# Kernel tuning notes

Hardware: AMD Instinct MI355X
Metric: run time of the kernel (lower is better)

The kernel has to match this reference:

```python
import jax, jax.numpy as jnp
import numpy as np

N = 100000      # num_assets (nodes)
E = 1600000     # edges (avg degree 16)
D_IN, D_H, D_OUT = 128, 64, 64


def gcn_conv(x, W, b, src, dst, dinv):
    """PyG-style GCNConv: h = D^{-1/2}(A+I)D^{-1/2} (x @ W) + b.
    Self-loop contribution handled analytically (norm = dinv[i]^2)."""
    h = x @ W                                   # [N, out]
    norm = dinv[src] * dinv[dst]                # [E]
    agg = jax.ops.segment_sum(h[src] * norm[:, None], dst, num_segments=N)
    agg = agg + h * (dinv * dinv)[:, None]      # self-loops
    return agg + b


def setup_inputs() -> dict:
    key = jax.random.key(0)
    ks = jax.random.split(key, 10)
    x = jax.random.normal(ks[0], (N, D_IN), dtype=jnp.float32)
    edge_index = jax.random.randint(ks[1], (2, E), 0, N, dtype=jnp.int64)
    s = 0.1
    W1 = jax.random.normal(ks[2], (D_IN, D_H), dtype=jnp.float32) * s
    b1 = jnp.zeros((D_H,), dtype=jnp.float32)
    W2 = jax.random.normal(ks[3], (D_H, D_H), dtype=jnp.float32) * s
    b2 = jnp.zeros((D_H,), dtype=jnp.float32)
    W3 = jax.random.normal(ks[4], (D_H, D_OUT), dtype=jnp.float32) * s
    b3 = jnp.zeros((D_OUT,), dtype=jnp.float32)
    Wa = jax.random.normal(ks[5], (D_OUT, D_OUT), dtype=jnp.float32) * s  # torch Linear weight [out,in]
    ba = jnp.zeros((D_OUT,), dtype=jnp.float32)
    q = jax.random.normal(ks[6], (D_OUT, 1), dtype=jnp.float32)
    battn = jax.random.normal(ks[7], (1,), dtype=jnp.float32)
    return {"x": x, "edge_index": edge_index, "W1": W1, "b1": b1,
            "W2": W2, "b2": b2, "W3": W3, "b3": b3,
            "Wa": Wa, "ba": ba, "q": q, "battn": battn}


def reference(x, edge_index, W1, b1, W2, b2, W3, b3, Wa, ba, q, battn):
    src, dst = edge_index[0], edge_index[1]
    # degree of A + I (computed once, shared by all layers)
    deg = jax.ops.segment_sum(jnp.ones((E,), dtype=x.dtype), dst, num_segments=N) + 1.0
    dinv = jax.lax.rsqrt(deg)

    h = jax.nn.relu(gcn_conv(x, W1, b1, src, dst, dinv))
    h = jax.nn.relu(gcn_conv(h, W2, b2, src, dst, dinv))
    z_context = gcn_conv(h, W3, b3, src, dst, dinv)          # [N, D_OUT]

    attn_scores = jnp.tanh(z_context @ Wa.T + ba) @ q + battn  # [N, 1]
    attn = jax.nn.softmax(attn_scores, axis=0)                 # softmax over nodes
    global_context = jnp.sum(attn * z_context, axis=0)         # [D_OUT]
    return (z_context, global_context)
```

## Files before the change

kernel.cpp:

```cpp
#include <hip/hip_runtime.h>
#include <hip/hip_fp16.h>
#include <math.h>
#include <stdint.h>


__global__ void detect_i64_kernel(const int* __restrict__ ei, int* __restrict__ flag) {
    int t = threadIdx.x;
    int bad = 0;
#pragma unroll
    for (int j = 0; j < 4; j++)
        bad |= (ei[1 + 2 * (t * 4 + j)] != 0);
    unsigned long long m = __ballot(bad);
    if (t == 0) *flag = (m == 0ull) ? 1 : 0;
}

__global__ void fill_kernel(const void* __restrict__ ei, const int* __restrict__ flag,
                            int* __restrict__ cnt, int* __restrict__ buckets,
                            int CAP, int E, int lo, int hi) {
    int e = blockIdx.x * 256 + threadIdx.x;
    if (e >= E) return;
    int is64 = *flag;
    int d = is64 ? (int)((const long long*)ei)[E + e] : ((const int*)ei)[E + e];
    if (d < lo || d >= hi) return;
    int s = is64 ? (int)((const long long*)ei)[e] : ((const int*)ei)[e];
    int pos = atomicAdd(&cnt[d], 1);
    if (pos < CAP) buckets[(size_t)d * CAP + pos] = s;
}

__global__ void dinv_kernel(const int* __restrict__ cnt, float* __restrict__ dinv, int N) {
    int i = blockIdx.x * 256 + threadIdx.x;
    if (i < N) dinv[i] = rsqrtf((float)cnt[i] + 1.0f);
}

template <int K, bool PRE>
__global__ __launch_bounds__(256) void gemm64(const float* __restrict__ in,
                                              const float* __restrict__ Wg,
                                              const float* __restrict__ bias,
                                              const float* __restrict__ dinv,
                                              __half* __restrict__ outh, int nrows) {
    constexpr int KQ = K / 4;
    __shared__ float Wt[64 * K];
    __shared__ float bl[K];
    const int t  = threadIdx.x;
    const int rb = blockIdx.x * 64;

    for (int qidx = t; qidx < K * 16; qidx += 256) {
        int k  = qidx >> 4;
        int c0 = (qidx & 15) << 2;
        float4 v = *(const float4*)(Wg + k * 64 + c0);
        float vv[4] = {v.x, v.y, v.z, v.w};
#pragma unroll
        for (int j = 0; j < 4; j++) {
            int c  = c0 + j;
            int kq = (k >> 2) ^ ((c >> 2) & 7);
            Wt[(c * KQ + kq) * 4 + (k & 3)] = vv[j];
        }
    }
    if (PRE) {
        for (int idx = t; idx < K; idx += 256) bl[idx] = bias[idx];
    }
    __syncthreads();

    const int tc = t & 15;
    const int tr = t >> 4;
    int rowi[4];
#pragma unroll
    for (int i = 0; i < 4; i++) {
        int r = rb + tr * 4 + i;
        rowi[i] = (r < nrows) ? r : (nrows - 1);
    }

    float acc[4][4];
#pragma unroll
    for (int i = 0; i < 4; i++)
#pragma unroll
        for (int j = 0; j < 4; j++) acc[i][j] = 0.f;

#pragma unroll 2
    for (int kb = 0; kb < KQ; ++kb) {
        float4 a[4];
#pragma unroll
        for (int i = 0; i < 4; i++)
            a[i] = *(const float4*)(in + (size_t)rowi[i] * K + (kb << 2));
        if (PRE) {
            float4 bb = *(const float4*)(bl + (kb << 2));
#pragma unroll
            for (int i = 0; i < 4; i++) {
                a[i].x = fmaxf(a[i].x + bb.x, 0.f);
                a[i].y = fmaxf(a[i].y + bb.y, 0.f);
                a[i].z = fmaxf(a[i].z + bb.z, 0.f);
                a[i].w = fmaxf(a[i].w + bb.w, 0.f);
            }
        }
        float4 w[4];
#pragma unroll
        for (int j = 0; j < 4; j++) {
            int c = tc * 4 + j;
            w[j] = *(const float4*)(&Wt[(c * KQ + (kb ^ ((c >> 2) & 7))) * 4]);
        }
#pragma unroll
        for (int i = 0; i < 4; i++)
#pragma unroll
            for (int j = 0; j < 4; j++)
                acc[i][j] += a[i].x * w[j].x + a[i].y * w[j].y +
                             a[i].z * w[j].z + a[i].w * w[j].w;
    }
#pragma unroll
    for (int i = 0; i < 4; i++) {
        int r = rb + tr * 4 + i;
        if (r < nrows) {
            float dd = dinv[r];
            __half2 p0 = __floats2half2_rn(acc[i][0] * dd, acc[i][1] * dd);
            __half2 p1 = __floats2half2_rn(acc[i][2] * dd, acc[i][3] * dd);
            uint2 pk;
            pk.x = *(unsigned int*)&p0;
            pk.y = *(unsigned int*)&p1;
            *(uint2*)(outh + (size_t)r * 64 + tc * 4) = pk;
        }
    }
}

template <bool BIAS>
__global__ __launch_bounds__(256) void gather64(const __half* __restrict__ hs,
                                                const int* __restrict__ cnt,
                                                const int* __restrict__ buckets,
                                                int CAP,
                                                const float* __restrict__ bias,
                                                float* __restrict__ out, int N) {
    const int wid = (blockIdx.x * 256 + threadIdx.x) >> 6;
    if (wid >= N) return;
    const int lane = threadIdx.x & 63;
    const int g    = lane >> 4;
    const int q    = lane & 15;

    const int deg  = cnt[wid];
    const int degc = min(deg, CAP);
    const int* bk  = buckets + (size_t)wid * CAP;
    const int pm   = degc - 1;

    float4 acc = make_float4(0.f, 0.f, 0.f, 0.f);
    if (g == 0) {
        uint2 v = *(const uint2*)(hs + (size_t)wid * 64 + q * 4);
        float2 f0 = __half22float2(*(__half2*)&v.x);
        float2 f1 = __half22float2(*(__half2*)&v.y);
        acc = make_float4(f0.x, f0.y, f1.x, f1.y);
    }

    for (int base = 0; base < degc; base += 16) {
        int i0 = base + g;
        int i1 = i0 + 4;
        int i2 = i0 + 8;
        int i3 = i0 + 12;
        int s0 = bk[i0 <= pm ? i0 : pm];
        int s1 = bk[i1 <= pm ? i1 : pm];
        int s2 = bk[i2 <= pm ? i2 : pm];
        int s3 = bk[i3 <= pm ? i3 : pm];
        uint2 v0 = *(const uint2*)(hs + (size_t)s0 * 64 + q * 4);
        uint2 v1 = *(const uint2*)(hs + (size_t)s1 * 64 + q * 4);
        uint2 v2 = *(const uint2*)(hs + (size_t)s2 * 64 + q * 4);
        uint2 v3 = *(const uint2*)(hs + (size_t)s3 * 64 + q * 4);
        float m0 = (i0 <= pm) ? 1.f : 0.f;
        float m1 = (i1 <= pm) ? 1.f : 0.f;
        float m2 = (i2 <= pm) ? 1.f : 0.f;
        float m3 = (i3 <= pm) ? 1.f : 0.f;
        float2 a0 = __half22float2(*(__half2*)&v0.x), b0 = __half22float2(*(__half2*)&v0.y);
        float2 a1 = __half22float2(*(__half2*)&v1.x), b1 = __half22float2(*(__half2*)&v1.y);
        float2 a2 = __half22float2(*(__half2*)&v2.x), b2 = __half22float2(*(__half2*)&v2.y);
        float2 a3 = __half22float2(*(__half2*)&v3.x), b3 = __half22float2(*(__half2*)&v3.y);
        acc.x = fmaf(m0, a0.x, acc.x); acc.y = fmaf(m0, a0.y, acc.y);
        acc.z = fmaf(m0, b0.x, acc.z); acc.w = fmaf(m0, b0.y, acc.w);
        acc.x = fmaf(m1, a1.x, acc.x); acc.y = fmaf(m1, a1.y, acc.y);
        acc.z = fmaf(m1, b1.x, acc.z); acc.w = fmaf(m1, b1.y, acc.w);
        acc.x = fmaf(m2, a2.x, acc.x); acc.y = fmaf(m2, a2.y, acc.y);
        acc.z = fmaf(m2, b2.x, acc.z); acc.w = fmaf(m2, b2.y, acc.w);
        acc.x = fmaf(m3, a3.x, acc.x); acc.y = fmaf(m3, a3.y, acc.y);
        acc.z = fmaf(m3, b3.x, acc.z); acc.w = fmaf(m3, b3.y, acc.w);
    }
    acc.x += __shfl_xor(acc.x, 16); acc.y += __shfl_xor(acc.y, 16);
    acc.z += __shfl_xor(acc.z, 16); acc.w += __shfl_xor(acc.w, 16);
    acc.x += __shfl_xor(acc.x, 32); acc.y += __shfl_xor(acc.y, 32);
    acc.z += __shfl_xor(acc.z, 32); acc.w += __shfl_xor(acc.w, 32);

    if (g == 0) {
        float dd = rsqrtf((float)deg + 1.0f);
        float4 o = make_float4(acc.x * dd, acc.y * dd, acc.z * dd, acc.w * dd);
        if (BIAS) {
            float4 b = *(const float4*)(bias + q * 4);
            o.x += b.x; o.y += b.y; o.z += b.z; o.w += b.w;
        }
        *(float4*)(out + (size_t)wid * 64 + q * 4) = o;
    }
}

__device__ __forceinline__ float fast_tanh(float x) {
    float e = __expf(2.f * x);
    return 1.f - 2.f * __builtin_amdgcn_rcpf(e + 1.f);
}

__global__ __launch_bounds__(256) void scoregc_kernel(const float* __restrict__ z,
                                                      const float* __restrict__ Wa,
                                                      const float* __restrict__ ba,
                                                      const float* __restrict__ q,
                                                      const float* __restrict__ battn,
                                                      float* __restrict__ blockmax,
                                                      float* __restrict__ bsumE,
                                                      float* __restrict__ bpart, int N) {
    __shared__ float Wl[64 * 64];
    __shared__ float es[256];
    __shared__ float red[256];
    __shared__ float gp[4][64];
    int t = threadIdx.x;
    for (int idx = t * 4; idx < 64 * 64; idx += 1024)
        *(float4*)(Wl + idx) = *(const float4*)(Wa + idx);
    __syncthreads();

    int i = blockIdx.x * 256 + t;
    float sc = -1e30f;
    if (i < N) {
        float zi[64];
#pragma unroll
        for (int kq = 0; kq < 16; kq++) {
            float4 v = *(const float4*)(z + (size_t)i * 64 + kq * 4);
            zi[kq * 4 + 0] = v.x; zi[kq * 4 + 1] = v.y;
            zi[kq * 4 + 2] = v.z; zi[kq * 4 + 3] = v.w;
        }
        float s = battn[0];
        for (int j = 0; j < 64; j++) {
            float t0 = ba[j], t1 = 0.f, t2 = 0.f, t3 = 0.f;
#pragma unroll
            for (int kq = 0; kq < 16; kq++) {
                float4 w4 = *(const float4*)(Wl + j * 64 + kq * 4);
                t0 = fmaf(zi[kq * 4 + 0], w4.x, t0);
                t1 = fmaf(zi[kq * 4 + 1], w4.y, t1);
                t2 = fmaf(zi[kq * 4 + 2], w4.z, t2);
                t3 = fmaf(zi[kq * 4 + 3], w4.w, t3);
            }
            s += fast_tanh((t0 + t1) + (t2 + t3)) * q[j];
        }
        sc = s;
    }
    red[t] = sc;
    __syncthreads();
    for (int off = 128; off > 0; off >>= 1) {
        if (t < off) red[t] = fmaxf(red[t], red[t + off]);
        __syncthreads();
    }
    float m_b = red[0];
    __syncthreads();
    float e = (i < N) ? __expf(sc - m_b) : 0.f;
    es[t] = e;
    red[t] = e;
    __syncthreads();
    for (int off = 128; off > 0; off >>= 1) {
        if (t < off) red[t] += red[t + off];
        __syncthreads();
    }
    if (t == 0) { bsumE[blockIdx.x] = red[0]; blockmax[blockIdx.x] = m_b; }
    int f = t & 63, g = t >> 6;
    int base = blockIdx.x * 256;
    float a = 0.f;
    for (int n = 0; n < 64; n++) {
        int idx = base + g * 64 + n;
        if (idx < N) a = fmaf(es[g * 64 + n], z[(size_t)idx * 64 + f], a);
    }
    gp[g][f] = a;
    __syncthreads();
    if (g == 0) bpart[(size_t)blockIdx.x * 64 + f] = gp[0][f] + gp[1][f] + gp[2][f] + gp[3][f];
}

__global__ __launch_bounds__(1024) void final3_kernel(const float* __restrict__ blockmax,
                                                      const float* __restrict__ bsumE,
                                                      const float* __restrict__ bpart,
                                                      int NB, float* __restrict__ outg) {
    __shared__ float sm[1024];
    __shared__ float se[1024];
    __shared__ float sa[16][64];
    int t = threadIdx.x;
    float m = -1e30f;
    for (int b = t; b < NB; b += 1024) m = fmaxf(m, blockmax[b]);
    sm[t] = m;
    __syncthreads();
    for (int off = 512; off > 0; off >>= 1) {
        if (t < off) sm[t] = fmaxf(sm[t], sm[t + off]);
        __syncthreads();
    }
    float M = sm[0];

    float es = 0.f;
    for (int b = t; b < NB; b += 1024) es += bsumE[b] * __expf(blockmax[b] - M);
    se[t] = es;
    __syncthreads();
    for (int off = 512; off > 0; off >>= 1) {
        if (t < off) se[t] += se[t + off];
        __syncthreads();
    }

    int f = t & 63, c = t >> 6;
    float a = 0.f;
    for (int b = c; b < NB; b += 16)
        a += bpart[(size_t)b * 64 + f] * __expf(blockmax[b] - M);
    sa[c][f] = a;
    __syncthreads();
    for (int off = 8; off > 0; off >>= 1) {
        if (c < off) sa[c][f] += sa[c + off][f];
        __syncthreads();
    }
    if (c == 0) outg[f] = sa[0][f] / se[0];
}

extern "C" void kernel_launch(void* const* d_in, const int* in_sizes, int n_in,
                              void* d_out, int out_size, void* d_ws, size_t ws_size,
                              hipStream_t stream) {
    const float* x     = (const float*)d_in[0];
    const void*  ei    = d_in[1];
    const float* W1    = (const float*)d_in[2];
    const float* b1    = (const float*)d_in[3];
    const float* W2    = (const float*)d_in[4];
    const float* b2    = (const float*)d_in[5];
    const float* W3    = (const float*)d_in[6];
    const float* b3    = (const float*)d_in[7];
    const float* Wa    = (const float*)d_in[8];
    const float* ba    = (const float*)d_in[9];
    const float* q     = (const float*)d_in[10];
    const float* battn = (const float*)d_in[11];

    const int N = in_sizes[0] / 128;
    const int E = in_sizes[1] / 2;

    float*  ws       = (float*)d_ws;
    float*  dinv     = ws;
    __half* H        = (__half*)(ws + N);
    float*  blockmax = ws + N + (size_t)32 * N;
    float*  bsumE    = blockmax + 512;
    float*  bpart    = bsumE + 512;
    int*    flag     = (int*)(bpart + 512 * 64);
    int*    cnt      = flag + 4;
    int*    buckets  = cnt + N;

    size_t fixed_bytes = (size_t)((char*)buckets - (char*)d_ws);
    size_t rem = (ws_size > fixed_bytes) ? (ws_size - fixed_bytes) : 0;
    size_t cap_fit = rem / ((size_t)N * sizeof(int));
    int CAP = (int)(cap_fit < 64 ? cap_fit : 64);
    if (CAP < 8) CAP = 8;

    float* Z    = (float*)d_out;
    float* outg = Z + (size_t)N * 64;

    hipMemsetAsync(cnt, 0, (size_t)N * sizeof(int), stream);
    detect_i64_kernel<<<1, 64, 0, stream>>>((const int*)ei, flag);

    const int NP = 4;
    const int rng = (N + NP - 1) / NP;
    for (int p = 0; p < NP; ++p) {
        int lo = p * rng;
        int hi = (p == NP - 1) ? N : lo + rng;
        fill_kernel<<<(E + 255) / 256, 256, 0, stream>>>(ei, flag, cnt, buckets,
                                                         CAP, E, lo, hi);
    }
    dinv_kernel<<<(N + 255) / 256, 256, 0, stream>>>(cnt, dinv, N);

    const int gb = (N + 63) / 64;
    const int ag = (int)(((long long)N * 64 + 255) / 256);
    const int NB = (N + 255) / 256;

    gemm64<128, false><<<gb, 256, 0, stream>>>(x, W1, nullptr, dinv, H, N);
    gather64<false><<<ag, 256, 0, stream>>>(H, cnt, buckets, CAP, nullptr, Z, N);

    gemm64<64, true><<<gb, 256, 0, stream>>>(Z, W2, b1, dinv, H, N);
    gather64<false><<<ag, 256, 0, stream>>>(H, cnt, buckets, CAP, nullptr, Z, N);

    gemm64<64, true><<<gb, 256, 0, stream>>>(Z, W3, b2, dinv, H, N);
    gather64<true><<<ag, 256, 0, stream>>>(H, cnt, buckets, CAP, b3, Z, N);

    scoregc_kernel<<<NB, 256, 0, stream>>>(Z, Wa, ba, q, battn,
                                           blockmax, bsumE, bpart, N);
    final3_kernel<<<1, 1024, 0, stream>>>(blockmax, bsumE, bpart, NB, outg);
}
```

Before: 367.7 us.

## Shrink attention score kernel to one wavefront per block with shuffle reductions

The attention-score and partial global-context kernel now runs 64-thread blocks (one wavefront) and replaces the shared-memory tree reductions and barriers with cross-lane shuffles. Wa is read straight from global memory, where the uniform address should hit cache, instead of being staged in LDS. This removes LDS staging and __syncthreads overhead, but quadruples the number of per-block partials that the final single-block reduction must combine. The workspace is enlarged to hold the extra partials.

```diff
diff --git a/kernel.cpp b/kernel.cpp
--- a/kernel.cpp
+++ b/kernel.cpp
@@ -197,39 +197,39 @@
     return 1.f - 2.f * __builtin_amdgcn_rcpf(e + 1.f);
 }
 
-__global__ __launch_bounds__(256) void scoregc_kernel(const float* __restrict__ z,
-                                                      const float* __restrict__ Wa,
-                                                      const float* __restrict__ ba,
-                                                      const float* __restrict__ q,
-                                                      const float* __restrict__ battn,
-                                                      float* __restrict__ blockmax,
-                                                      float* __restrict__ bsumE,
-                                                      float* __restrict__ bpart, int N) {
-    __shared__ float Wl[64 * 64];
-    __shared__ float es[256];
-    __shared__ float red[256];
-    __shared__ float gp[4][64];
-    int t = threadIdx.x;
-    for (int idx = t * 4; idx < 64 * 64; idx += 1024)
-        *(float4*)(Wl + idx) = *(const float4*)(Wa + idx);
-    __syncthreads();
-
-    int i = blockIdx.x * 256 + t;
-    float sc = -1e30f;
-    if (i < N) {
-        float zi[64];
+__global__ __launch_bounds__(64) void scoregc_kernel(const float* __restrict__ z,
+                                                     const float* __restrict__ Wa,
+                                                     const float* __restrict__ ba,
+                                                     const float* __restrict__ q,
+                                                     const float* __restrict__ battn,
+                                                     float* __restrict__ blockmax,
+                                                     float* __restrict__ bsumE,
+                                                     float* __restrict__ bpart, int N) {
+    const int t = threadIdx.x;
+    const int i = blockIdx.x * 64 + t;
+    const bool act = (i < N);
+
+    float zi[64];
+    if (act) {
 #pragma unroll
         for (int kq = 0; kq < 16; kq++) {
             float4 v = *(const float4*)(z + (size_t)i * 64 + kq * 4);
             zi[kq * 4 + 0] = v.x; zi[kq * 4 + 1] = v.y;
             zi[kq * 4 + 2] = v.z; zi[kq * 4 + 3] = v.w;
         }
+    } else {
+#pragma unroll
+        for (int k = 0; k < 64; k++) zi[k] = 0.f;
+    }
+
+    float sc = -1e30f;
+    {
         float s = battn[0];
         for (int j = 0; j < 64; j++) {
             float t0 = ba[j], t1 = 0.f, t2 = 0.f, t3 = 0.f;
 #pragma unroll
             for (int kq = 0; kq < 16; kq++) {
-                float4 w4 = *(const float4*)(Wl + j * 64 + kq * 4);
+                float4 w4 = *(const float4*)(Wa + j * 64 + kq * 4);
                 t0 = fmaf(zi[kq * 4 + 0], w4.x, t0);
                 t1 = fmaf(zi[kq * 4 + 1], w4.y, t1);
                 t2 = fmaf(zi[kq * 4 + 2], w4.z, t2);
@@ -237,35 +237,27 @@
             }
             s += fast_tanh((t0 + t1) + (t2 + t3)) * q[j];
         }
-        sc = s;
-    }
-    red[t] = sc;
-    __syncthreads();
-    for (int off = 128; off > 0; off >>= 1) {
-        if (t < off) red[t] = fmaxf(red[t], red[t + off]);
-        __syncthreads();
-    }
-    float m_b = red[0];
-    __syncthreads();
-    float e = (i < N) ? __expf(sc - m_b) : 0.f;
-    es[t] = e;
-    red[t] = e;
-    __syncthreads();
-    for (int off = 128; off > 0; off >>= 1) {
-        if (t < off) red[t] += red[t + off];
-        __syncthreads();
-    }
-    if (t == 0) { bsumE[blockIdx.x] = red[0]; blockmax[blockIdx.x] = m_b; }
-    int f = t & 63, g = t >> 6;
-    int base = blockIdx.x * 256;
+        if (act) sc = s;
+    }
+
+    float m = sc;
+#pragma unroll
+    for (int off = 32; off > 0; off >>= 1) m = fmaxf(m, __shfl_xor(m, off));
+    float e = act ? __expf(sc - m) : 0.f;
+    float se = e;
+#pragma unroll
+    for (int off = 32; off > 0; off >>= 1) se += __shfl_xor(se, off);
+    if (t == 0) { blockmax[blockIdx.x] = m; bsumE[blockIdx.x] = se; }
+
+    const int base = blockIdx.x * 64;
     float a = 0.f;
     for (int n = 0; n < 64; n++) {
-        int idx = base + g * 64 + n;
-        if (idx < N) a = fmaf(es[g * 64 + n], z[(size_t)idx * 64 + f], a);
-    }
-    gp[g][f] = a;
-    __syncthreads();
-    if (g == 0) bpart[(size_t)blockIdx.x * 64 + f] = gp[0][f] + gp[1][f] + gp[2][f] + gp[3][f];
+        float en = __shfl(e, n);
+        int idx = base + n;
+        idx = (idx < N) ? idx : (N - 1);
+        a = fmaf(en, z[(size_t)idx * 64 + t], a);
+    }
+    bpart[(size_t)blockIdx.x * 64 + t] = a;
 }
 
 __global__ __launch_bounds__(1024) void final3_kernel(const float* __restrict__ blockmax,
@@ -331,9 +323,9 @@
     float*  dinv     = ws;
     __half* H        = (__half*)(ws + N);
     float*  blockmax = ws + N + (size_t)32 * N;
-    float*  bsumE    = blockmax + 512;
-    float*  bpart    = bsumE + 512;
-    int*    flag     = (int*)(bpart + 512 * 64);
+    float*  bsumE    = blockmax + 2048;
+    float*  bpart    = bsumE + 2048;
+    int*    flag     = (int*)(bpart + 2048 * 64);
     int*    cnt      = flag + 4;
     int*    buckets  = cnt + N;
 
@@ -361,7 +353,7 @@
 
     const int gb = (N + 63) / 64;
     const int ag = (int)(((long long)N * 64 + 255) / 256);
-    const int NB = (N + 255) / 256;
+    const int NBW = (N + 63) / 64;
 
     gemm64<128, false><<<gb, 256, 0, stream>>>(x, W1, nullptr, dinv, H, N);
     gather64<false><<<ag, 256, 0, stream>>>(H, cnt, buckets, CAP, nullptr, Z, N);
@@ -372,7 +364,7 @@
     gemm64<64, true><<<gb, 256, 0, stream>>>(Z, W3, b2, dinv, H, N);
     gather64<true><<<ag, 256, 0, stream>>>(H, cnt, buckets, CAP, b3, Z, N);
 
-    scoregc_kernel<<<NB, 256, 0, stream>>>(Z, Wa, ba, q, battn,
+    scoregc_kernel<<<NBW, 64, 0, stream>>>(Z, Wa, ba, q, battn,
                                            blockmax, bsumE, bpart, N);
-    final3_kernel<<<1, 1024, 0, stream>>>(blockmax, bsumE, bpart, NB, outg);
-}
+    final3_kernel<<<1, 1024, 0, stream>>>(blockmax, bsumE, bpart, NBW, outg);
+}
```

Measured after the change: 380.1 us. 1.03x slower.
